# Optimization experiments

Measured on AMD Instinct MI355X. Metric: run time of the kernel, lower is better.

Reference implementation:

```python
import jax, jax.numpy as jnp
import numpy as np

B, N, D = 2, 2048, 1024
H = 16                      # num_heads, head_dim = 64
E, K, CF = 4, 2, 1.0        # num_experts, top_k, capacity_factor
MLP_H = int(D * 4.0)        # dense Mlp hidden (mlp_ratio=4.0)
MOE_H = int(D * 0.25)       # expert hidden (hard-coded dim*0.25 in source)


def setup_inputs() -> dict:
    key = jax.random.key(0)
    ks = jax.random.split(key, 12)
    r = lambda k, shp, s=0.02: jax.random.normal(k, shp, jnp.float32) * s
    return dict(
        x=jax.random.normal(ks[0], (B, N, D), jnp.float32),
        noise=jax.random.normal(ks[1], (B, N, E), jnp.float32),
        ln1_g=jnp.ones((D,), jnp.float32), ln1_b=jnp.zeros((D,), jnp.float32),
        ln2_g=jnp.ones((D,), jnp.float32), ln2_b=jnp.zeros((D,), jnp.float32),
        w_qkv=r(ks[2], (3 * D, D)),
        w_proj=r(ks[3], (D, D)), b_proj=jnp.zeros((D,), jnp.float32),
        w_route=r(ks[4], (D, E), 0.05), b_route=jnp.zeros((E,), jnp.float32),
        w_noise=r(ks[5], (D, E), 0.05), b_noise=jnp.zeros((E,), jnp.float32),
        we1=r(ks[6], (E, D, MOE_H)), be1=jnp.zeros((E, MOE_H), jnp.float32),
        we2=r(ks[7], (E, MOE_H, D)), be2=jnp.zeros((E, D), jnp.float32),
        w_mlp1=r(ks[8], (D, MLP_H)), b_mlp1=jnp.zeros((MLP_H,), jnp.float32),
        w_mlp2=r(ks[9], (MLP_H, D)), b_mlp2=jnp.zeros((D,), jnp.float32),
    )


def _ln(x, g, b, eps=1e-5):
    mu = x.mean(-1, keepdims=True)
    var = ((x - mu) ** 2).mean(-1, keepdims=True)
    return (x - mu) * jax.lax.rsqrt(var + eps) * g + b


def _gelu(x):
    return jax.nn.gelu(x, approximate=False)  # torch nn.GELU default (erf)


def reference(x, noise, ln1_g, ln1_b, ln2_g, ln2_b, w_qkv, w_proj, b_proj,
              w_route, b_route, w_noise, b_noise, we1, be1, we2, be2,
              w_mlp1, b_mlp1, w_mlp2, b_mlp2):
    Bs, Ns, Ds = x.shape
    hd = Ds // H
    # --- attention branch ---
    x1 = _ln(x, ln1_g, ln1_b)
    qkv = (x1 @ w_qkv.T).reshape(Bs, Ns, 3, H, hd).transpose(2, 0, 3, 1, 4)
    q, k, v = qkv[0] * (hd ** -0.5), qkv[1], qkv[2]
    attn = jax.nn.softmax(jnp.einsum('bhnd,bhmd->bhnm', q, k), axis=-1)
    ao = jnp.einsum('bhnm,bhmd->bhnd', attn, v).transpose(0, 2, 1, 3).reshape(Bs, Ns, Ds)
    x = x + (ao @ w_proj.T + b_proj)
    # --- shared norm for mlp + moe ---
    x2 = _ln(x, ln2_g, ln2_b)
    # --- noisy top-k router ---
    logits = x2 @ w_route + b_route                  # [B,N,E]
    noisy = logits + noise * jax.nn.softplus(x2 @ w_noise + b_noise)
    topv, topi = jax.lax.top_k(noisy, K)             # [B,N,K]
    probs = jax.nn.softmax(topv, axis=-1)            # softmax over sparse logits == softmax over top-k
    T = Bs * Ns
    flat_x = x2.reshape(T, Ds)
    fidx = topi.reshape(T, K)
    rows = jnp.arange(T)[:, None]
    gate = jnp.zeros((T, E), noisy.dtype).at[rows, fidx].set(probs.reshape(T, K))
    capacity = int(T * K / E * CF)
    # --- capacity-limited dispatch / expert MLP / combine ---
    def dispatch(eid, W1, b1, W2, b2):
        mask = jnp.any(fidx == eid, axis=-1)                     # [T]
        order = jnp.argsort(jnp.logical_not(mask))               # stable: selected tokens first, in token order
        sel = order[:capacity]                                   # [C]
        valid = mask[sel].astype(flat_x.dtype)
        h = _gelu(flat_x[sel] @ W1 + b1)
        out = h @ W2 + b2
        w = gate[sel, eid] * valid
        return sel, out * w[:, None]
    sel, outw = jax.vmap(dispatch)(jnp.arange(E), we1, be1, we2, be2)   # [E,C], [E,C,D]
    moe = jnp.zeros_like(flat_x).at[sel.reshape(-1)].add(outw.reshape(-1, Ds)).reshape(Bs, Ns, Ds)
    # --- dense mlp branch ---
    mlp = _gelu(x2 @ w_mlp1 + b_mlp1) @ w_mlp2 + b_mlp2
    return x + mlp + moe
```

## Files before the change

### kernel.cpp

```cpp
#include <hip/hip_runtime.h>
#include <hip/hip_bf16.h>
#include <math.h>

typedef __bf16 bf16;
typedef __bf16 bf16x4 __attribute__((ext_vector_type(4)));
typedef __bf16 bf16x8 __attribute__((ext_vector_type(8)));
typedef float  f32x4  __attribute__((ext_vector_type(4)));
typedef short  s16x4  __attribute__((ext_vector_type(4)));

#define T_TOK 4096
#define DIM   1024
#define NHEAD 16
#define SEQ   2048
#define NEXP  4
#define CAP   2048
#define MLPH  4096
#define MOEH  256

__device__ __forceinline__ float gelu_exact(float v) {
    return 0.5f * v * (1.f + erff(v * 0.70710678118654752f));
}

struct HL { bf16 h, l; };
__device__ __forceinline__ HL split2(float v) {
    HL r; r.h = (bf16)v; r.l = (bf16)(v - (float)r.h); return r;
}

__device__ __forceinline__ float fast_exp2(float x) {
#if __has_builtin(__builtin_amdgcn_exp2f)
    return __builtin_amdgcn_exp2f(x);
#else
    return exp2f(x);
#endif
}

__device__ __forceinline__ f32x4 mfma16(bf16x4 a, bf16x4 b, f32x4 c) {
    return __builtin_amdgcn_mfma_f32_16x16x16bf16_1k(
        __builtin_bit_cast(s16x4, a), __builtin_bit_cast(s16x4, b), c, 0, 0, 0);
}

__device__ __forceinline__ void gload16(const bf16* gptr, bf16* lptr) {
    __builtin_amdgcn_global_load_lds(
        (const __attribute__((address_space(1))) unsigned int*)gptr,
        (__attribute__((address_space(3))) unsigned int*)lptr,
        16, 0, 0);
}

__global__ __launch_bounds__(256)
void ln_split_kernel(const float* __restrict__ x, const float* __restrict__ g,
                     const float* __restrict__ b, bf16* __restrict__ oh, bf16* __restrict__ ol) {
    int wave = threadIdx.x >> 6, lane = threadIdx.x & 63;
    long t = (long)blockIdx.x * 4 + wave;
    const float* xr = x + t * DIM;
    float v[16];
    #pragma unroll
    for (int i = 0; i < 16; i++) v[i] = xr[i * 64 + lane];
    float s = 0.f, s2 = 0.f;
    #pragma unroll
    for (int i = 0; i < 16; i++) { s += v[i]; s2 += v[i] * v[i]; }
    #pragma unroll
    for (int m = 1; m < 64; m <<= 1) { s += __shfl_xor(s, m); s2 += __shfl_xor(s2, m); }
    float mu  = s * (1.f / DIM);
    float var = s2 * (1.f / DIM) - mu * mu;
    float rs  = 1.f / sqrtf(var + 1e-5f);
    #pragma unroll
    for (int i = 0; i < 16; i++) {
        int d = i * 64 + lane;
        HL sp = split2((v[i] - mu) * rs * g[d] + b[d]);
        oh[t * DIM + d] = sp.h; ol[t * DIM + d] = sp.l;
    }
}

__global__ __launch_bounds__(256)
void ln_kernel(const float* __restrict__ x, const float* __restrict__ g,
               const float* __restrict__ b, bf16* __restrict__ out) {
    int wave = threadIdx.x >> 6, lane = threadIdx.x & 63;
    long t = (long)blockIdx.x * 4 + wave;
    const float* xr = x + t * DIM;
    float v[16];
    #pragma unroll
    for (int i = 0; i < 16; i++) v[i] = xr[i * 64 + lane];
    float s = 0.f, s2 = 0.f;
    #pragma unroll
    for (int i = 0; i < 16; i++) { s += v[i]; s2 += v[i] * v[i]; }
    #pragma unroll
    for (int m = 1; m < 64; m <<= 1) { s += __shfl_xor(s, m); s2 += __shfl_xor(s2, m); }
    float mu  = s * (1.f / DIM);
    float var = s2 * (1.f / DIM) - mu * mu;
    float rs  = 1.f / sqrtf(var + 1e-5f);
    #pragma unroll
    for (int i = 0; i < 16; i++) {
        int d = i * 64 + lane;
        out[t * DIM + d] = (bf16)((v[i] - mu) * rs * g[d] + b[d]);
    }
}

__global__ __launch_bounds__(256)
void split_pair_kernel(const float* __restrict__ in, bf16* __restrict__ h, bf16* __restrict__ l) {
    long i0 = ((long)blockIdx.x * 256 + threadIdx.x) * 4;
    f32x4 v = *(const f32x4*)&in[i0];
    bf16x4 vh, vl;
    #pragma unroll
    for (int j = 0; j < 4; j++) { HL sp = split2(v[j]); vh[j] = sp.h; vl[j] = sp.l; }
    *(bf16x4*)&h[i0] = vh; *(bf16x4*)&l[i0] = vl;
}

__global__ __launch_bounds__(256)
void transpose_conv_kernel(const float* __restrict__ in, bf16* __restrict__ out, int R, int C) {
    __shared__ bf16 tile[32][33];
    long bo = (long)blockIdx.z * R * C;
    in += bo; out += bo;
    int c0 = blockIdx.x * 32, r0 = blockIdx.y * 32;
    int tx = threadIdx.x & 31, ty = threadIdx.x >> 5;
    #pragma unroll
    for (int i = 0; i < 32; i += 8)
        tile[ty + i][tx] = (bf16)in[(long)(r0 + ty + i) * C + c0 + tx];
    __syncthreads();
    #pragma unroll
    for (int i = 0; i < 32; i += 8)
        out[(long)(c0 + ty + i) * R + r0 + tx] = tile[tx][ty + i];
}

__global__ __launch_bounds__(256)
void gemm_qkv(const bf16* __restrict__ Ah_g, const bf16* __restrict__ Al_g,
              const bf16* __restrict__ Bh_g, const bf16* __restrict__ Bl_g,
              bf16* __restrict__ Qh_g, bf16* __restrict__ Ql_g,
              bf16* __restrict__ Kh_g, bf16* __restrict__ Kl_g,
              bf16* __restrict__ VtH, bf16* __restrict__ VtL) {
    const int K = DIM;
    __shared__ alignas(16) bf16 Ah[8192], Al[8192], Bh[8192], Bl[8192];
    int tid = threadIdx.x;
    int wave = tid >> 6, lane = tid & 63;
    int l16 = lane & 15, l4 = lane >> 4;
    int wr = (wave >> 1) * 64, wc = (wave & 1) * 64;
    int row0 = blockIdx.y * 128, col0 = blockIdx.x * 128;
    int colb = (lane & 7) * 8;
    f32x4 acc[4][4] = {};
    for (int k0 = 0; k0 < K; k0 += 64) {
        #pragma unroll
        for (int p = 0; p < 4; p++) {
            int rl = p * 32 + wave * 8 + (lane >> 3);
            int lb = p * 2048 + wave * 512;
            gload16(&Ah_g[(long)(row0 + rl) * K + k0 + colb], &Ah[lb]);
            gload16(&Al_g[(long)(row0 + rl) * K + k0 + colb], &Al[lb]);
            gload16(&Bh_g[(long)(col0 + rl) * K + k0 + colb], &Bh[lb]);
            gload16(&Bl_g[(long)(col0 + rl) * K + k0 + colb], &Bl[lb]);
        }
        __syncthreads();
        #pragma unroll
        for (int ks = 0; ks < 2; ks++) {
            bf16x8 ah[4], al[4], bh[4], bl[4];
            #pragma unroll
            for (int i = 0; i < 4; i++) {
                ah[i] = *(const bf16x8*)&Ah[(wr + i*16 + l16)*64 + ks*32 + l4*8];
                al[i] = *(const bf16x8*)&Al[(wr + i*16 + l16)*64 + ks*32 + l4*8];
            }
            #pragma unroll
            for (int j = 0; j < 4; j++) {
                bh[j] = *(const bf16x8*)&Bh[(wc + j*16 + l16)*64 + ks*32 + l4*8];
                bl[j] = *(const bf16x8*)&Bl[(wc + j*16 + l16)*64 + ks*32 + l4*8];
            }
            #pragma unroll
            for (int i = 0; i < 4; i++)
                #pragma unroll
                for (int j = 0; j < 4; j++) {
                    acc[i][j] = __builtin_amdgcn_mfma_f32_16x16x32_bf16(ah[i], bh[j], acc[i][j], 0, 0, 0);
                    acc[i][j] = __builtin_amdgcn_mfma_f32_16x16x32_bf16(ah[i], bl[j], acc[i][j], 0, 0, 0);
                    acc[i][j] = __builtin_amdgcn_mfma_f32_16x16x32_bf16(al[i], bh[j], acc[i][j], 0, 0, 0);
                }
        }
        __syncthreads();
    }
    if (col0 < 2048) {
        bf16* oh = (col0 < 1024) ? Qh_g : Kh_g;
        bf16* ol = (col0 < 1024) ? Ql_g : Kl_g;
        float qscale = (col0 < 1024) ? 0.18033688011112043f : 1.0f;
        #pragma unroll
        for (int i = 0; i < 4; i++)
            #pragma unroll
            for (int r = 0; r < 4; r++) {
                int t = row0 + wr + i * 16 + l4 * 4 + r;
                int bq = t >> 11, s = t & 2047;
                #pragma unroll
                for (int j = 0; j < 4; j++) {
                    int col = (col0 + wc + j * 16 + l16) & 1023;
                    int hh = col >> 6, dl = col & 63;
                    long o = ((long)(bq * NHEAD + hh) * SEQ + s) * 64 + dl;
                    HL sp = split2(acc[i][j][r] * qscale);
                    oh[o] = sp.h; ol[o] = sp.l;
                }
            }
    } else {
        #pragma unroll
        for (int i = 0; i < 4; i++) {
            int s0 = row0 + wr + i * 16 + l4 * 4;
            int b = s0 >> 11, sl = s0 & 2047;
            #pragma unroll
            for (int j = 0; j < 4; j++) {
                int d = col0 - 2048 + wc + j * 16 + l16;
                int h = d >> 6, dl = d & 63;
                long base = ((long)(b * NHEAD + h) * 64 + dl) * SEQ + sl;
                bf16x4 vh, vl;
                #pragma unroll
                for (int r = 0; r < 4; r++) { HL sp = split2(acc[i][j][r]); vh[r] = sp.h; vl[r] = sp.l; }
                *(bf16x4*)&VtH[base] = vh;
                *(bf16x4*)&VtL[base] = vl;
            }
        }
    }
}

__device__ __forceinline__ bf16x8 sw_frag(const bf16* arr, int row, int cc) {
    return *(const bf16x8*)&arr[row * 64 + ((cc ^ (row & 7)) * 8)];
}
__device__ __forceinline__ bf16x4 sw_frag64(const bf16* arr, int row, int cc, int sub) {
    return *(const bf16x4*)&arr[row * 64 + ((cc ^ (row & 7)) * 8) + sub * 4];
}

__global__ __launch_bounds__(256, 4)
void flash_attn(const bf16* __restrict__ Qh_g, const bf16* __restrict__ Ql_g,
                const bf16* __restrict__ Kh_g, const bf16* __restrict__ Kl_g,
                const bf16* __restrict__ VtH_g, const bf16* __restrict__ VtL_g,
                bf16* __restrict__ aoh, bf16* __restrict__ aol) {
    __shared__ alignas(16) bf16 Kh[4096], Kl[4096], Vth[4096], Vtl[4096];
    int tid = threadIdx.x;
    int wave = tid >> 6, lane = tid & 63;
    int l16 = lane & 15, l4 = lane >> 4;
    int bid = blockIdx.x;
    int bh = bid & 31;
    int b = bh >> 4, h = bh & 15;
    int q0 = (bid >> 5) * 64;

    bf16x8 qfh[2], qfl[2];
    {
        const bf16* qh = Qh_g + ((long)bh * SEQ + q0 + wave * 16 + l16) * 64;
        const bf16* ql = Ql_g + ((long)bh * SEQ + q0 + wave * 16 + l16) * 64;
        #pragma unroll
        for (int ks = 0; ks < 2; ks++) {
            qfh[ks] = *(const bf16x8*)&qh[ks * 32 + l4 * 8];
            qfl[ks] = *(const bf16x8*)&ql[ks * 32 + l4 * 8];
        }
    }
    int r8 = lane >> 3;
    int swc = ((lane & 7) ^ r8) * 8;
    float m_s = -1e30f, l_s = 0.f;
    f32x4 accO[4] = {};

    for (int c0 = 0; c0 < SEQ; c0 += 64) {
        __syncthreads();
        {
            const bf16* kh = Kh_g + ((long)bh * SEQ + c0) * 64;
            const bf16* kl = Kl_g + ((long)bh * SEQ + c0) * 64;
            const bf16* vh = VtH_g + (long)bh * 64 * SEQ + c0;
            const bf16* vl = VtL_g + (long)bh * 64 * SEQ + c0;
            #pragma unroll
            for (int p = 0; p < 2; p++) {
                int R0 = wave * 16 + p * 8;
                int row = R0 + r8;
                gload16(&kh[(long)row * 64 + swc], &Kh[R0 * 64]);
                gload16(&kl[(long)row * 64 + swc], &Kl[R0 * 64]);
                gload16(&vh[(long)row * SEQ + swc], &Vth[R0 * 64]);
                gload16(&vl[(long)row * SEQ + swc], &Vtl[R0 * 64]);
            }
        }
        __syncthreads();
        f32x4 st[4] = {};
        #pragma unroll
        for (int ks = 0; ks < 2; ks++) {
            #pragma unroll
            for (int i = 0; i < 4; i++) {
                bf16x8 akh = sw_frag(Kh, i * 16 + l16, ks * 4 + l4);
                bf16x8 akl = sw_frag(Kl, i * 16 + l16, ks * 4 + l4);
                st[i] = __builtin_amdgcn_mfma_f32_16x16x32_bf16(akh, qfh[ks], st[i], 0, 0, 0);
                st[i] = __builtin_amdgcn_mfma_f32_16x16x32_bf16(akl, qfh[ks], st[i], 0, 0, 0);
                st[i] = __builtin_amdgcn_mfma_f32_16x16x32_bf16(akh, qfl[ks], st[i], 0, 0, 0);
            }
        }
        float mx = st[0][0];
        #pragma unroll
        for (int i = 0; i < 4; i++)
            #pragma unroll
            for (int r = 0; r < 4; r++) mx = fmaxf(mx, st[i][r]);
        mx = fmaxf(mx, __shfl_xor(mx, 16));
        mx = fmaxf(mx, __shfl_xor(mx, 32));
        if (!__all(mx <= m_s + 8.f)) {
            float mnew = fmaxf(m_s, mx);
            float alpha = fast_exp2(m_s - mnew);
            l_s *= alpha;
            #pragma unroll
            for (int i = 0; i < 4; i++)
                #pragma unroll
                for (int r = 0; r < 4; r++) accO[i][r] *= alpha;
            m_s = mnew;
        }
        float psum = 0.f;
        bf16x4 ph[4], pl[4];
        #pragma unroll
        for (int kb = 0; kb < 4; kb++)
            #pragma unroll
            for (int r = 0; r < 4; r++) {
                float pv = fast_exp2(st[kb][r] - m_s);
                psum += pv;
                HL sp = split2(pv);
                ph[kb][r] = sp.h; pl[kb][r] = sp.l;
            }
        psum += __shfl_xor(psum, 16);
        psum += __shfl_xor(psum, 32);
        l_s += psum;
        #pragma unroll
        for (int kb = 0; kb < 4; kb++) {
            int cc = kb * 2 + (l4 >> 1), sub = l4 & 1;
            #pragma unroll
            for (int i = 0; i < 4; i++) {
                bf16x4 avh = sw_frag64(Vth, i * 16 + l16, cc, sub);
                bf16x4 avl = sw_frag64(Vtl, i * 16 + l16, cc, sub);
                accO[i] = mfma16(avh, ph[kb], accO[i]);
                accO[i] = mfma16(avh, pl[kb], accO[i]);
                accO[i] = mfma16(avl, ph[kb], accO[i]);
            }
        }
    }
    float inv = 1.f / l_s;
    int q = q0 + wave * 16 + l16;
    #pragma unroll
    for (int i = 0; i < 4; i++) {
        bf16x4 oh4, ol4;
        #pragma unroll
        for (int r = 0; r < 4; r++) { HL sp = split2(accO[i][r] * inv); oh4[r] = sp.h; ol4[r] = sp.l; }
        long o = ((long)(b * SEQ + q)) * DIM + h * 64 + i * 16 + l4 * 4;
        *(bf16x4*)&aoh[o] = oh4;
        *(bf16x4*)&aol[o] = ol4;
    }
}

__global__ __launch_bounds__(256)
void gemm_proj(const bf16* __restrict__ Ah_g, const bf16* __restrict__ Al_g,
               const bf16* __restrict__ Bh_g, const bf16* __restrict__ Bl_g,
               const float* __restrict__ bias, const float* __restrict__ res,
               float* __restrict__ C, int N, int K) {
    __shared__ alignas(16) bf16 Ah[8192], Al[8192], Bh[8192], Bl[8192];
    int tid = threadIdx.x;
    int wave = tid >> 6, lane = tid & 63;
    int l16 = lane & 15, l4 = lane >> 4;
    int wr = (wave >> 1) * 64, wc = (wave & 1) * 64;
    int row0 = blockIdx.y * 128, col0 = blockIdx.x * 128;
    int colb = (lane & 7) * 8;
    f32x4 acc[4][4] = {};
    for (int k0 = 0; k0 < K; k0 += 64) {
        #pragma unroll
        for (int p = 0; p < 4; p++) {
            int rl = p * 32 + wave * 8 + (lane >> 3);
            int lb = p * 2048 + wave * 512;
            gload16(&Ah_g[(long)(row0 + rl) * K + k0 + colb], &Ah[lb]);
            gload16(&Al_g[(long)(row0 + rl) * K + k0 + colb], &Al[lb]);
            gload16(&Bh_g[(long)(col0 + rl) * K + k0 + colb], &Bh[lb]);
            gload16(&Bl_g[(long)(col0 + rl) * K + k0 + colb], &Bl[lb]);
        }
        __syncthreads();
        #pragma unroll
        for (int ks = 0; ks < 2; ks++) {
            bf16x8 ah[4], al[4], bh[4], bl[4];
            #pragma unroll
            for (int i = 0; i < 4; i++) {
                ah[i] = *(const bf16x8*)&Ah[(wr + i*16 + l16)*64 + ks*32 + l4*8];
                al[i] = *(const bf16x8*)&Al[(wr + i*16 + l16)*64 + ks*32 + l4*8];
            }
            #pragma unroll
            for (int j = 0; j < 4; j++) {
                bh[j] = *(const bf16x8*)&Bh[(wc + j*16 + l16)*64 + ks*32 + l4*8];
                bl[j] = *(const bf16x8*)&Bl[(wc + j*16 + l16)*64 + ks*32 + l4*8];
            }
            #pragma unroll
            for (int i = 0; i < 4; i++)
                #pragma unroll
                for (int j = 0; j < 4; j++) {
                    acc[i][j] = __builtin_amdgcn_mfma_f32_16x16x32_bf16(ah[i], bh[j], acc[i][j], 0, 0, 0);
                    acc[i][j] = __builtin_amdgcn_mfma_f32_16x16x32_bf16(ah[i], bl[j], acc[i][j], 0, 0, 0);
                    acc[i][j] = __builtin_amdgcn_mfma_f32_16x16x32_bf16(al[i], bh[j], acc[i][j], 0, 0, 0);
                }
        }
        __syncthreads();
    }
    #pragma unroll
    for (int i = 0; i < 4; i++)
        #pragma unroll
        for (int r = 0; r < 4; r++) {
            int grow = row0 + wr + i * 16 + l4 * 4 + r;
            #pragma unroll
            for (int j = 0; j < 4; j++) {
                int gcol = col0 + wc + j * 16 + l16;
                long o = (long)grow * N + gcol;
                C[o] = acc[i][j][r] + bias[gcol] + res[o];
            }
        }
}

template<bool BIAS, bool GELU, bool GATHER, int OUT_MODE>
__global__ __launch_bounds__(256)
void gemm_bt(const bf16* __restrict__ A, const bf16* __restrict__ Bt,
             const float* __restrict__ bias,
             bf16* __restrict__ Cbf, float* __restrict__ Cf,
             const int* __restrict__ rowmap, const float* __restrict__ roww,
             int M, int N, int K,
             long eA, long eB, long ebias, long eMap, long eC) {
    int ez = blockIdx.z;
    A += (long)ez * eA; Bt += (long)ez * eB;
    if (BIAS) bias += (long)ez * ebias;
    if (GATHER || OUT_MODE == 3) rowmap += (long)ez * eMap;
    if (OUT_MODE == 3) roww += (long)ez * eMap;
    if (OUT_MODE == 0) Cbf += (long)ez * eC;

    __shared__ alignas(16) bf16 As[8192];
    __shared__ alignas(16) bf16 Bs[8192];
    int tid = threadIdx.x;
    int wave = tid >> 6, lane = tid & 63;
    int l16 = lane & 15, l4 = lane >> 4;
    int wr = (wave >> 1) * 64, wc = (wave & 1) * 64;
    int row0 = blockIdx.y * 128, col0 = blockIdx.x * 128;
    int colb = (lane & 7) * 8;

    long arow[4];
    #pragma unroll
    for (int p = 0; p < 4; p++) {
        long gr = row0 + p * 32 + wave * 8 + (lane >> 3);
        if (GATHER) gr = rowmap[gr];
        arow[p] = gr;
    }
    f32x4 acc[4][4] = {};
    for (int k0 = 0; k0 < K; k0 += 64) {
        #pragma unroll
        for (int p = 0; p < 4; p++) {
            int rl = p * 32 + wave * 8 + (lane >> 3);
            int lb = p * 2048 + wave * 512;
            gload16(&A[arow[p] * K + k0 + colb], &As[lb]);
            gload16(&Bt[(long)(col0 + rl) * K + k0 + colb], &Bs[lb]);
        }
        __syncthreads();
        #pragma unroll
        for (int ks = 0; ks < 2; ks++) {
            bf16x8 af[4], bfr[4];
            #pragma unroll
            for (int i = 0; i < 4; i++) af[i]  = *(const bf16x8*)&As[(wr + i*16 + l16)*64 + ks*32 + l4*8];
            #pragma unroll
            for (int j = 0; j < 4; j++) bfr[j] = *(const bf16x8*)&Bs[(wc + j*16 + l16)*64 + ks*32 + l4*8];
            #pragma unroll
            for (int i = 0; i < 4; i++)
                #pragma unroll
                for (int j = 0; j < 4; j++)
                    acc[i][j] = __builtin_amdgcn_mfma_f32_16x16x32_bf16(af[i], bfr[j], acc[i][j], 0, 0, 0);
        }
        __syncthreads();
    }
    #pragma unroll
    for (int i = 0; i < 4; i++)
        #pragma unroll
        for (int r = 0; r < 4; r++) {
            int grow = row0 + wr + i * 16 + l4 * 4 + r;
            int st = 0; float sw = 0.f;
            if (OUT_MODE == 3) { st = rowmap[grow]; sw = roww[grow]; }
            #pragma unroll
            for (int j = 0; j < 4; j++) {
                int gcol = col0 + wc + j * 16 + l16;
                float v = acc[i][j][r];
                if (BIAS) v += bias[gcol];
                if (GELU) v = gelu_exact(v);
                if (OUT_MODE == 0) {
                    Cbf[(long)grow * N + gcol] = (bf16)v;
                } else if (OUT_MODE == 2) {
                    long o = (long)grow * N + gcol;
                    Cf[o] += v;
                } else {
                    atomicAdd(&Cf[(long)st * N + gcol], sw * v);
                }
            }
        }
}

__global__ __launch_bounds__(256)
void routing_kernel(const float* __restrict__ xres, const float* __restrict__ g,
                    const float* __restrict__ b, const float* __restrict__ w_route,
                    const float* __restrict__ b_route, const float* __restrict__ w_noise,
                    const float* __restrict__ b_noise, const float* __restrict__ noise,
                    int* __restrict__ topi, float* __restrict__ topp) {
    int wave = threadIdx.x >> 6, lane = threadIdx.x & 63;
    long t = (long)blockIdx.x * 4 + wave;
    const float* xr = xres + t * DIM;
    float v[16];
    #pragma unroll
    for (int i = 0; i < 16; i++) v[i] = xr[i * 64 + lane];
    float s = 0.f, s2 = 0.f;
    #pragma unroll
    for (int i = 0; i < 16; i++) { s += v[i]; s2 += v[i] * v[i]; }
    #pragma unroll
    for (int m = 1; m < 64; m <<= 1) { s += __shfl_xor(s, m); s2 += __shfl_xor(s2, m); }
    float mu  = s * (1.f / DIM);
    float var = s2 * (1.f / DIM) - mu * mu;
    float rs  = 1.f / sqrtf(var + 1e-5f);
    float accr[4] = {0.f,0.f,0.f,0.f}, accn[4] = {0.f,0.f,0.f,0.f};
    #pragma unroll
    for (int i = 0; i < 16; i++) {
        int d = i * 64 + lane;
        float n = (v[i] - mu) * rs * g[d] + b[d];
        #pragma unroll
        for (int e = 0; e < 4; e++) {
            accr[e] += n * w_route[d * 4 + e];
            accn[e] += n * w_noise[d * 4 + e];
        }
    }
    #pragma unroll
    for (int e = 0; e < 4; e++)
        #pragma unroll
        for (int m = 1; m < 64; m <<= 1) {
            accr[e] += __shfl_xor(accr[e], m);
            accn[e] += __shfl_xor(accn[e], m);
        }
    if (lane == 0) {
        float nz[4];
        #pragma unroll
        for (int e = 0; e < 4; e++) {
            float logit = accr[e] + b_route[e];
            float si = accn[e] + b_noise[e];
            float sp = si > 0.f ? si + log1pf(expf(-si)) : log1pf(expf(si));
            nz[e] = logit + noise[t * 4 + e] * sp;
        }
        int i1 = 0;
        #pragma unroll
        for (int e = 1; e < 4; e++) if (nz[e] > nz[i1]) i1 = e;
        int i2 = -1; float v2 = -1e30f;
        #pragma unroll
        for (int e = 0; e < 4; e++) if (e != i1 && nz[e] > v2) { v2 = nz[e]; i2 = e; }
        float ex = expf(v2 - nz[i1]);
        topi[t * 2]     = i1; topi[t * 2 + 1] = i2;
        topp[t * 2]     = 1.f / (1.f + ex);
        topp[t * 2 + 1] = ex / (1.f + ex);
    }
}

__global__ __launch_bounds__(256)
void dispatch_kernel(const int* __restrict__ topi, const float* __restrict__ topp,
                     int* __restrict__ sel, float* __restrict__ wgt) {
    int e = threadIdx.x >> 6, lane = threadIdx.x & 63;
    int cnt = 0;
    for (int c = 0; c < T_TOK; c += 64) {
        int t = c + lane;
        int i0 = topi[t * 2], i1 = topi[t * 2 + 1];
        bool m = (i0 == e) || (i1 == e);
        unsigned long long bal = __ballot(m);
        int pos = cnt + __popcll(bal & ((1ull << lane) - 1ull));
        if (m && pos < CAP) {
            sel[e * CAP + pos] = t;
            wgt[e * CAP + pos] = (i0 == e) ? topp[t * 2] : topp[t * 2 + 1];
        }
        cnt += (int)__popcll(bal);
    }
    if (cnt > CAP) cnt = CAP;
    for (int pos = cnt + lane; pos < CAP; pos += 64) {
        sel[e * CAP + pos] = 0;
        wgt[e * CAP + pos] = 0.f;
    }
}

extern "C" void kernel_launch(void* const* d_in, const int* in_sizes, int n_in,
                              void* d_out, int out_size, void* d_ws, size_t ws_size,
                              hipStream_t stream) {
    (void)in_sizes; (void)n_in; (void)out_size; (void)ws_size;
    const float* x       = (const float*)d_in[0];
    const float* noise   = (const float*)d_in[1];
    const float* ln1_g   = (const float*)d_in[2];
    const float* ln1_b   = (const float*)d_in[3];
    const float* ln2_g   = (const float*)d_in[4];
    const float* ln2_b   = (const float*)d_in[5];
    const float* w_qkv   = (const float*)d_in[6];
    const float* w_proj  = (const float*)d_in[7];
    const float* b_proj  = (const float*)d_in[8];
    const float* w_route = (const float*)d_in[9];
    const float* b_route = (const float*)d_in[10];
    const float* w_noise = (const float*)d_in[11];
    const float* b_noise = (const float*)d_in[12];
    const float* we1     = (const float*)d_in[13];
    const float* be1     = (const float*)d_in[14];
    const float* we2     = (const float*)d_in[15];
    const float* be2     = (const float*)d_in[16];
    const float* w_mlp1  = (const float*)d_in[17];
    const float* b_mlp1  = (const float*)d_in[18];
    const float* w_mlp2  = (const float*)d_in[19];
    const float* b_mlp2  = (const float*)d_in[20];
    float* d_outf = (float*)d_out;

    const size_t MB = 1024 * 1024;
    char* ws = (char*)d_ws;
    bf16* x1h = (bf16*)(ws);
    bf16* x1l = (bf16*)(ws + 8 * MB);
    bf16* aoh = (bf16*)(ws);
    bf16* aol = (bf16*)(ws + 8 * MB);
    bf16* w_mlp1T = (bf16*)(ws);
    bf16* w_mlp2T = (bf16*)(ws + 8 * MB);
    bf16* wqkvh = (bf16*)(ws + 16 * MB);
    bf16* wqkvl = (bf16*)(ws + 22 * MB);
    bf16* we1T  = (bf16*)(ws + 16 * MB);
    bf16* we2T  = (bf16*)(ws + 18 * MB);
    bf16* h_e   = (bf16*)(ws + 20 * MB);
    bf16* wprojh = (bf16*)(ws + 28 * MB);
    bf16* wprojl = (bf16*)(ws + 30 * MB);
    bf16* Qh = (bf16*)(ws + 32 * MB);
    bf16* Ql = (bf16*)(ws + 40 * MB);
    bf16* Kh = (bf16*)(ws + 48 * MB);
    bf16* Kl = (bf16*)(ws + 56 * MB);
    bf16* h_mlp = (bf16*)(ws + 32 * MB);
    bf16*  VtH  = (bf16*)(ws + 64 * MB);
    bf16*  VtL  = (bf16*)(ws + 72 * MB);
    bf16*  x2b  = (bf16*)(ws + 64 * MB);
    int*   topi = (int*)(ws + 72 * MB);
    float* topp = (float*)(ws + 72 * MB + 32768);
    int*   sel  = (int*)(ws + 72 * MB + 65536);
    float* wgt  = (float*)(ws + 72 * MB + 98304);

    ln_split_kernel<<<T_TOK/4, 256, 0, stream>>>(x, ln1_g, ln1_b, x1h, x1l);
    split_pair_kernel<<<(3*DIM*DIM)/1024, 256, 0, stream>>>(w_qkv, wqkvh, wqkvl);
    split_pair_kernel<<<(DIM*DIM)/1024,   256, 0, stream>>>(w_proj, wprojh, wprojl);

    gemm_qkv<<<dim3(3*DIM/128, T_TOK/128), 256, 0, stream>>>(
        x1h, x1l, wqkvh, wqkvl, Qh, Ql, Kh, Kl, VtH, VtL);

    flash_attn<<<dim3(32 * (SEQ/64)), 256, 0, stream>>>(Qh, Ql, Kh, Kl, VtH, VtL, aoh, aol);

    gemm_proj<<<dim3(DIM/128, T_TOK/128), 256, 0, stream>>>(
        aoh, aol, wprojh, wprojl, b_proj, x, d_outf, DIM, DIM);

    ln_kernel<<<T_TOK/4, 256, 0, stream>>>(d_outf, ln2_g, ln2_b, x2b);
    routing_kernel<<<T_TOK/4, 256, 0, stream>>>(d_outf, ln2_g, ln2_b, w_route, b_route,
                                                w_noise, b_noise, noise, topi, topp);
    dispatch_kernel<<<1, 256, 0, stream>>>(topi, topp, sel, wgt);

    transpose_conv_kernel<<<dim3(MLPH/32, DIM/32, 1),    256, 0, stream>>>(w_mlp1, w_mlp1T, DIM, MLPH);
    transpose_conv_kernel<<<dim3(DIM/32, MLPH/32, 1),    256, 0, stream>>>(w_mlp2, w_mlp2T, MLPH, DIM);
    transpose_conv_kernel<<<dim3(MOEH/32, DIM/32, NEXP), 256, 0, stream>>>(we1, we1T, DIM, MOEH);
    transpose_conv_kernel<<<dim3(DIM/32, MOEH/32, NEXP), 256, 0, stream>>>(we2, we2T, MOEH, DIM);

    gemm_bt<true,true,false,0><<<dim3(MLPH/128, T_TOK/128), 256, 0, stream>>>(
        x2b, w_mlp1T, b_mlp1, h_mlp, nullptr, nullptr, nullptr, T_TOK, MLPH, DIM,
        0, 0, 0, 0, 0);
    gemm_bt<true,false,false,2><<<dim3(DIM/128, T_TOK/128), 256, 0, stream>>>(
        h_mlp, w_mlp2T, b_mlp2, nullptr, d_outf, nullptr, nullptr, T_TOK, DIM, MLPH,
        0, 0, 0, 0, 0);

    gemm_bt<true,true,true,0><<<dim3(MOEH/128, CAP/128, NEXP), 256, 0, stream>>>(
        x2b, we1T, be1, h_e, nullptr, sel, nullptr, CAP, MOEH, DIM,
        0, (long)MOEH*DIM, MOEH, CAP, (long)CAP*MOEH);
    gemm_bt<true,false,false,3><<<dim3(DIM/128, CAP/128, NEXP), 256, 0, stream>>>(
        h_e, we2T, be2, nullptr, d_outf, sel, wgt, CAP, DIM, MOEH,
        (long)CAP*MOEH, (long)DIM*MOEH, DIM, CAP, 0);
}
```

Measured before the change: 691.5 us.

## Double-buffer K/V tiles in flash attention with async prefetch and new V swizzle

Moves the flash attention K/V loop onto two LDS buffers, so the next tile's global-to-LDS loads are issued while the current tile is computed, with vmcnt waits and barriers in place of the old sync-load-sync pattern. It also changes the V^T layout written by the QKV GEMM (an XOR on the sequence index) and the LDS swizzle used to read V fragments, aiming to cut bank conflicts. s_setprio is raised around the MFMA sections. Doubling LDS lowers the occupancy hint from 4 to 2 blocks per CU, which costs latency hiding.

After: 692.4 us. About the same (+0.1%).

```diff
diff --git a/kernel.cpp b/kernel.cpp
--- a/kernel.cpp
+++ b/kernel.cpp
@@ -199,7 +199,7 @@
             for (int j = 0; j < 4; j++) {
                 int d = col0 - 2048 + wc + j * 16 + l16;
                 int h = d >> 6, dl = d & 63;
-                long base = ((long)(b * NHEAD + h) * 64 + dl) * SEQ + sl;
+                long base = ((long)(b * NHEAD + h) * 64 + dl) * SEQ + (sl ^ ((dl & 1) << 2));
                 bf16x4 vh, vl;
                 #pragma unroll
                 for (int r = 0; r < 4; r++) { HL sp = split2(acc[i][j][r]); vh[r] = sp.h; vl[r] = sp.l; }
@@ -213,16 +213,16 @@
 __device__ __forceinline__ bf16x8 sw_frag(const bf16* arr, int row, int cc) {
     return *(const bf16x8*)&arr[row * 64 + ((cc ^ (row & 7)) * 8)];
 }
-__device__ __forceinline__ bf16x4 sw_frag64(const bf16* arr, int row, int cc, int sub) {
-    return *(const bf16x4*)&arr[row * 64 + ((cc ^ (row & 7)) * 8) + sub * 4];
-}
-
-__global__ __launch_bounds__(256, 4)
+__device__ __forceinline__ bf16x4 v_frag(const bf16* arr, int d, int q) {
+    return *(const bf16x4*)&arr[d * 64 + ((q ^ (d & 15)) * 4)];
+}
+
+__global__ __launch_bounds__(256, 2)
 void flash_attn(const bf16* __restrict__ Qh_g, const bf16* __restrict__ Ql_g,
                 const bf16* __restrict__ Kh_g, const bf16* __restrict__ Kl_g,
                 const bf16* __restrict__ VtH_g, const bf16* __restrict__ VtL_g,
                 bf16* __restrict__ aoh, bf16* __restrict__ aol) {
-    __shared__ alignas(16) bf16 Kh[4096], Kl[4096], Vth[4096], Vtl[4096];
+    __shared__ alignas(16) bf16 KhS[2][4096], KlS[2][4096], VhS[2][4096], VlS[2][4096];
     int tid = threadIdx.x;
     int wave = tid >> 6, lane = tid & 63;
     int l16 = lane & 15, l4 = lane >> 4;
@@ -242,40 +242,44 @@
         }
     }
     int r8 = lane >> 3;
-    int swc = ((lane & 7) ^ r8) * 8;
+    int c8 = lane & 7;
+    const bf16* kh_g = Kh_g + (long)bh * SEQ * 64;
+    const bf16* kl_g = Kl_g + (long)bh * SEQ * 64;
+    const bf16* vh_g = VtH_g + (long)bh * 64 * SEQ;
+    const bf16* vl_g = VtL_g + (long)bh * 64 * SEQ;
+
     float m_s = -1e30f, l_s = 0.f;
     f32x4 accO[4] = {};
 
-    for (int c0 = 0; c0 < SEQ; c0 += 64) {
-        __syncthreads();
-        {
-            const bf16* kh = Kh_g + ((long)bh * SEQ + c0) * 64;
-            const bf16* kl = Kl_g + ((long)bh * SEQ + c0) * 64;
-            const bf16* vh = VtH_g + (long)bh * 64 * SEQ + c0;
-            const bf16* vl = VtL_g + (long)bh * 64 * SEQ + c0;
-            #pragma unroll
-            for (int p = 0; p < 2; p++) {
-                int R0 = wave * 16 + p * 8;
-                int row = R0 + r8;
-                gload16(&kh[(long)row * 64 + swc], &Kh[R0 * 64]);
-                gload16(&kl[(long)row * 64 + swc], &Kl[R0 * 64]);
-                gload16(&vh[(long)row * SEQ + swc], &Vth[R0 * 64]);
-                gload16(&vl[(long)row * SEQ + swc], &Vtl[R0 * 64]);
-            }
-        }
-        __syncthreads();
+    auto stage = [&](int c0, int bsel) {
+        #pragma unroll
+        for (int p = 0; p < 2; p++) {
+            int R0 = wave * 16 + p * 8;
+            int row = R0 + r8;
+            int ksw = (c8 ^ r8) * 8;
+            int vsw = (c8 ^ ((p * 4 + (r8 >> 1)) & 7)) * 8;
+            gload16(&kh_g[(long)(c0 + row) * 64 + ksw], &KhS[bsel][R0 * 64]);
+            gload16(&kl_g[(long)(c0 + row) * 64 + ksw], &KlS[bsel][R0 * 64]);
+            gload16(&vh_g[(long)row * SEQ + c0 + vsw], &VhS[bsel][R0 * 64]);
+            gload16(&vl_g[(long)row * SEQ + c0 + vsw], &VlS[bsel][R0 * 64]);
+        }
+    };
+
+    auto compute = [&](const bf16* KhT, const bf16* KlT, const bf16* VhT, const bf16* VlT) {
         f32x4 st[4] = {};
+        __builtin_amdgcn_s_setprio(1);
         #pragma unroll
         for (int ks = 0; ks < 2; ks++) {
             #pragma unroll
             for (int i = 0; i < 4; i++) {
-                bf16x8 akh = sw_frag(Kh, i * 16 + l16, ks * 4 + l4);
-                bf16x8 akl = sw_frag(Kl, i * 16 + l16, ks * 4 + l4);
+                bf16x8 akh = sw_frag(KhT, i * 16 + l16, ks * 4 + l4);
+                bf16x8 akl = sw_frag(KlT, i * 16 + l16, ks * 4 + l4);
                 st[i] = __builtin_amdgcn_mfma_f32_16x16x32_bf16(akh, qfh[ks], st[i], 0, 0, 0);
                 st[i] = __builtin_amdgcn_mfma_f32_16x16x32_bf16(akl, qfh[ks], st[i], 0, 0, 0);
                 st[i] = __builtin_amdgcn_mfma_f32_16x16x32_bf16(akh, qfl[ks], st[i], 0, 0, 0);
             }
         }
+        __builtin_amdgcn_s_setprio(0);
         float mx = st[0][0];
         #pragma unroll
         for (int i = 0; i < 4; i++)
@@ -307,19 +311,45 @@
         psum += __shfl_xor(psum, 16);
         psum += __shfl_xor(psum, 32);
         l_s += psum;
+        __builtin_amdgcn_s_setprio(1);
         #pragma unroll
         for (int kb = 0; kb < 4; kb++) {
-            int cc = kb * 2 + (l4 >> 1), sub = l4 & 1;
             #pragma unroll
             for (int i = 0; i < 4; i++) {
-                bf16x4 avh = sw_frag64(Vth, i * 16 + l16, cc, sub);
-                bf16x4 avl = sw_frag64(Vtl, i * 16 + l16, cc, sub);
+                bf16x4 avh = v_frag(VhT, i * 16 + l16, kb * 4 + l4);
+                bf16x4 avl = v_frag(VlT, i * 16 + l16, kb * 4 + l4);
                 accO[i] = mfma16(avh, ph[kb], accO[i]);
                 accO[i] = mfma16(avh, pl[kb], accO[i]);
                 accO[i] = mfma16(avl, ph[kb], accO[i]);
             }
         }
-    }
+        __builtin_amdgcn_s_setprio(0);
+    };
+
+    const int NT = SEQ / 64;
+    stage(0, 0);
+    #pragma unroll 1
+    for (int t = 0; t < NT; t += 2) {
+        stage((t + 1) * 64, 1);
+        asm volatile("s_waitcnt vmcnt(8)" ::: "memory");
+        __builtin_amdgcn_sched_barrier(0);
+        __builtin_amdgcn_s_barrier();
+        compute(KhS[0], KlS[0], VhS[0], VlS[0]);
+        asm volatile("" ::: "memory");
+        __builtin_amdgcn_s_barrier();
+        if (t + 2 < NT) {
+            stage((t + 2) * 64, 0);
+            asm volatile("s_waitcnt vmcnt(8)" ::: "memory");
+        } else {
+            asm volatile("s_waitcnt vmcnt(0)" ::: "memory");
+        }
+        __builtin_amdgcn_sched_barrier(0);
+        __builtin_amdgcn_s_barrier();
+        compute(KhS[1], KlS[1], VhS[1], VlS[1]);
+        asm volatile("" ::: "memory");
+        __builtin_amdgcn_s_barrier();
+    }
+
     float inv = 1.f / l_s;
     int q = q0 + wave * 16 + l16;
     #pragma unroll
```
